# Kernel optimization log

Hardware: AMD Instinct MI355X
Metric: run time of the kernel (lower is better)

The kernel has to match this reference:

```python
import jax, jax.numpy as jnp
import numpy as np

B, C, T, H, W = 2, 512, 8, 16, 16
NUM_HEADS = 8
HEAD_DIM = C // NUM_HEADS


def setup_inputs() -> dict:
    key = jax.random.key(0)
    ks = jax.random.split(key, 6)
    x = jax.random.normal(ks[0], (B, C, T, H, W), dtype=jnp.float32)
    # LayerNorm params
    ln_w = jnp.ones((C,), dtype=jnp.float32)
    ln_b = jnp.zeros((C,), dtype=jnp.float32)
    # 1x1x1 Conv3d == per-token linear; weight stored [out, in]
    w_qkv = jax.random.normal(ks[1], (3 * C, C), dtype=jnp.float32) * (1.0 / np.sqrt(C))
    b_qkv = jnp.zeros((3 * C,), dtype=jnp.float32)
    w_proj = jax.random.normal(ks[2], (C, C), dtype=jnp.float32) * (1.0 / np.sqrt(C))
    b_proj = jnp.zeros((C,), dtype=jnp.float32)
    return {"x": x, "ln_w": ln_w, "ln_b": ln_b, "w_qkv": w_qkv,
            "b_qkv": b_qkv, "w_proj": w_proj, "b_proj": b_proj}


def reference(x, ln_w, ln_b, w_qkv, b_qkv, w_proj, b_proj):
    Bx, Cx, Tx, Hx, Wx = x.shape
    N = Tx * Hx * Wx
    scale = HEAD_DIM ** -0.5

    # [B,C,T,H,W] -> [B,N,C]
    x_flat = jnp.transpose(x, (0, 2, 3, 4, 1)).reshape(Bx, N, Cx)

    # LayerNorm over channels
    mu = jnp.mean(x_flat, axis=-1, keepdims=True)
    var = jnp.var(x_flat, axis=-1, keepdims=True)
    x_flat = (x_flat - mu) * jax.lax.rsqrt(var + 1e-5) * ln_w + ln_b

    # QKV (1x1x1 conv == linear). Output channel layout: [3, heads, head_dim]
    qkv = jnp.einsum('bnc,oc->bno', x_flat, w_qkv) + b_qkv  # [B,N,3C]
    qkv = qkv.reshape(Bx, N, 3, NUM_HEADS, HEAD_DIM)
    qkv = jnp.transpose(qkv, (2, 0, 3, 1, 4))  # [3,B,heads,N,head_dim]
    q, k, v = qkv[0], qkv[1], qkv[2]

    attn = jnp.einsum('bhnd,bhmd->bhnm', q, k) * scale
    attn = jax.nn.softmax(attn, axis=-1)
    x_attn = jnp.einsum('bhnm,bhmd->bhnd', attn, v)  # [B,heads,N,head_dim]
    x_attn = jnp.transpose(x_attn, (0, 2, 1, 3)).reshape(Bx, N, Cx)

    # proj (1x1x1 conv == linear)
    x_attn = jnp.einsum('bnc,oc->bno', x_attn, w_proj) + b_proj

    # NOTE: residual is on the *normalized* x_flat (as in the original module)
    x_out = x_flat + x_attn
    x_out = x_out.reshape(Bx, Tx, Hx, Wx, Cx)
    return jnp.transpose(x_out, (0, 4, 1, 2, 3))  # [B,C,T,H,W]
```

## Files before the change

kernel.cpp:

```cpp
#include <hip/hip_runtime.h>
#include <hip/hip_bf16.h>

#define BB 2
#define CC 512
#define NN 2048
#define NHEADS 8
#define HDIM 64

typedef __attribute__((ext_vector_type(8))) __bf16 bf16x8;
typedef __attribute__((ext_vector_type(4))) __bf16 bf16x4;
typedef __attribute__((ext_vector_type(2))) __bf16 bf16x2;
typedef __attribute__((ext_vector_type(4))) float f32x4;

#define QSCALE 0.18033688f

__global__ __launch_bounds__(256) void ln_stats_kernel(
    const float* __restrict__ x, float* __restrict__ mu, float* __restrict__ rstd) {
  __shared__ float rs[16][16];
  __shared__ float rq[16][16];
  int tl = threadIdx.x & 15;
  int cg = threadIdx.x >> 4;
  int tok = blockIdx.x * 16 + tl;
  int b = tok >> 11;
  int n = tok & (NN - 1);
  const float* xp = x + (size_t)b * CC * NN + n;
  float s = 0.f, ss = 0.f;
  int c0 = cg * 32;
#pragma unroll 8
  for (int c = c0; c < c0 + 32; ++c) {
    float v = xp[(size_t)c * NN];
    s += v;
    ss += v * v;
  }
  rs[cg][tl] = s;
  rq[cg][tl] = ss;
  __syncthreads();
  if (threadIdx.x < 16) {
    int t = threadIdx.x;
    float S = 0.f, SS = 0.f;
#pragma unroll
    for (int gidx = 0; gidx < 16; ++gidx) {
      S += rs[gidx][t];
      SS += rq[gidx][t];
    }
    float m = S * (1.0f / CC);
    float var = SS * (1.0f / CC) - m * m;
    int tk = blockIdx.x * 16 + t;
    mu[tk] = m;
    rstd[tk] = rsqrtf(var + 1e-5f);
  }
}

__global__ __launch_bounds__(256) void ln_transpose_kernel(
    const float* __restrict__ x, const float* __restrict__ mu,
    const float* __restrict__ rstd, const float* __restrict__ lnw,
    const float* __restrict__ lnb, __bf16* __restrict__ xln_t) {
  __shared__ float Xs[64][68];
  int n0 = blockIdx.x * 64;
  int c0 = blockIdx.y * 64;
  int b = blockIdx.z;
  int tid = threadIdx.x;
#pragma unroll
  for (int l = 0; l < 4; ++l) {
    int e = tid + 256 * l;
    int row = e >> 4, c4 = e & 15;
    float4 v = *(const float4*)&x[((size_t)b * CC + c0 + row) * NN + n0 + c4 * 4];
    *(float4*)&Xs[row][c4 * 4] = v;
  }
  __syncthreads();
  int sr = tid >> 2;
  int sc = (tid & 3) * 16;
  int tok = b * NN + n0 + sr;
  float mun = mu[tok], rsn = rstd[tok];
  __bf16 outv[16];
#pragma unroll
  for (int j = 0; j < 16; ++j) {
    int c = c0 + sc + j;
    outv[j] = (__bf16)((Xs[sc + j][sr] - mun) * rsn * lnw[c] + lnb[c]);
  }
  __bf16* dst = &xln_t[((size_t)b * NN + n0 + sr) * CC + c0 + sc];
  *(bf16x8*)&dst[0] = *(bf16x8*)&outv[0];
  *(bf16x8*)&dst[8] = *(bf16x8*)&outv[8];
}

__global__ __launch_bounds__(256) void qkv_mfma_kernel(
    const __bf16* __restrict__ xln_t, const float* __restrict__ w,
    const float* __restrict__ bias, __bf16* __restrict__ qt,
    __bf16* __restrict__ kt, __bf16* __restrict__ vbf) {
  __shared__ __align__(16) __bf16 As[2][64][68];
  __shared__ __align__(16) __bf16 Bs[2][128][68];
  int n0 = blockIdx.x * 128;
  bool swap = blockIdx.y < 16;
  int m0 = swap ? blockIdx.y * 64 : 1024 + ((int)blockIdx.y - 16) * 64;
  int b = blockIdx.z;
  int tid = threadIdx.x;
  int wid = tid >> 6, lane = tid & 63;
  int g = lane >> 4, c = lane & 15;
  int wr = wid >> 1, wc = wid & 1;
  const __bf16* xln = xln_t + (size_t)b * NN * CC;
  int arow = tid >> 4, ac4 = tid & 15;
  int brow = tid >> 3, bc8 = tid & 7;

  float4 wA[4];
  bf16x8 xB[4];
  auto LOADREGS = [&](int k0) {
#pragma unroll
    for (int l = 0; l < 4; ++l)
      wA[l] = *(const float4*)&w[(size_t)(m0 + arow + 16 * l) * CC + k0 + ac4 * 4];
#pragma unroll
    for (int l = 0; l < 4; ++l)
      xB[l] = *(const bf16x8*)&xln[(size_t)(n0 + brow + 32 * l) * CC + k0 + bc8 * 8];
  };
  auto STORELDS = [&](int buf) {
#pragma unroll
    for (int l = 0; l < 4; ++l) {
      bf16x4 pk = {(__bf16)wA[l].x, (__bf16)wA[l].y, (__bf16)wA[l].z,
                   (__bf16)wA[l].w};
      *(bf16x4*)&As[buf][arow + 16 * l][ac4 * 4] = pk;
    }
#pragma unroll
    for (int l = 0; l < 4; ++l)
      *(bf16x8*)&Bs[buf][brow + 32 * l][bc8 * 8] = xB[l];
  };

  LOADREGS(0);
  STORELDS(0);
  __syncthreads();
  f32x4 acc[2][4] = {};
  for (int ktile = 0; ktile < 8; ++ktile) {
    int cur = ktile & 1;
    if (ktile < 7) LOADREGS((ktile + 1) * 64);
#pragma unroll
    for (int hh = 0; hh < 2; ++hh) {
      bf16x8 af[2], bfr[4];
#pragma unroll
      for (int mi = 0; mi < 2; ++mi)
        af[mi] = *(const bf16x8*)&As[cur][wr * 32 + mi * 16 + c][hh * 32 + g * 8];
#pragma unroll
      for (int nj = 0; nj < 4; ++nj)
        bfr[nj] = *(const bf16x8*)&Bs[cur][wc * 64 + nj * 16 + c][hh * 32 + g * 8];
      if (swap) {
#pragma unroll
        for (int mi = 0; mi < 2; ++mi)
#pragma unroll
          for (int nj = 0; nj < 4; ++nj)
            acc[mi][nj] = __builtin_amdgcn_mfma_f32_16x16x32_bf16(
                bfr[nj], af[mi], acc[mi][nj], 0, 0, 0);
      } else {
#pragma unroll
        for (int mi = 0; mi < 2; ++mi)
#pragma unroll
          for (int nj = 0; nj < 4; ++nj)
            acc[mi][nj] = __builtin_amdgcn_mfma_f32_16x16x32_bf16(
                af[mi], bfr[nj], acc[mi][nj], 0, 0, 0);
      }
    }
    if (ktile < 7) STORELDS(cur ^ 1);
    __syncthreads();
  }
  if (swap) {
    int obase = m0 + wr * 32;
    int sec = obase >> 9;
    int osec = obase & 511;
    int head = osec >> 6;
    int dbase = osec & 63;
    __bf16* dst = (sec == 0 ? qt : kt) + (size_t)(b * NHEADS + head) * NN * HDIM;
    float scl = (sec == 0) ? QSCALE : 1.0f;
#pragma unroll
    for (int mi = 0; mi < 2; ++mi) {
      float bo = bias[obase + mi * 16 + c];
      int d = dbase + mi * 16 + c;
#pragma unroll
      for (int nj = 0; nj < 4; ++nj)
#pragma unroll
        for (int r = 0; r < 4; ++r) {
          int n = n0 + wc * 64 + nj * 16 + 4 * g + r;
          dst[(size_t)n * HDIM + d] = (__bf16)((acc[mi][nj][r] + bo) * scl);
        }
    }
  } else {
#pragma unroll
    for (int mi = 0; mi < 2; ++mi)
#pragma unroll
      for (int r = 0; r < 4; ++r) {
        int o = m0 + wr * 32 + mi * 16 + 4 * g + r;
        int ch = o - 1024;
        float bo = bias[o];
#pragma unroll
        for (int nj = 0; nj < 4; ++nj) {
          int n = n0 + wc * 64 + nj * 16 + c;
          vbf[((size_t)b * CC + ch) * NN + n] = (__bf16)(acc[mi][nj][r] + bo);
        }
      }
  }
}

__global__ __launch_bounds__(256, 2) void attn_mfma_kernel(
    const __bf16* __restrict__ qt, const __bf16* __restrict__ ktg,
    const __bf16* __restrict__ vbf, __bf16* __restrict__ xa_t) {
  __shared__ __align__(16) __bf16 Kb[2][64][72];
  __shared__ __align__(16) __bf16 Vb[2][64][72];
  __shared__ __align__(16) __bf16 Ps[64][72];
  int tid = threadIdx.x;
  int wid = tid >> 6, lane = tid & 63;
  int g = lane >> 4, c = lane & 15;
  int n0 = blockIdx.x * 64;
  int h = blockIdx.y, b = blockIdx.z;
  int bh = b * NHEADS + h;
  const __bf16* qbase = qt + ((size_t)bh * NN + n0) * HDIM;
  const __bf16* kbase = ktg + (size_t)bh * NN * HDIM;
  const __bf16* vbase = vbf + ((size_t)b * CC + h * HDIM) * NN;

  int sr = tid >> 2, sc = (tid & 3) * 16;
  bf16x8 kr0 = *(const bf16x8*)(kbase + (size_t)sr * HDIM + sc);
  bf16x8 kr1 = *(const bf16x8*)(kbase + (size_t)sr * HDIM + sc + 8);
  bf16x8 vr0 = *(const bf16x8*)(vbase + (size_t)sr * NN + sc);
  bf16x8 vr1 = *(const bf16x8*)(vbase + (size_t)sr * NN + sc + 8);
  bf16x8 aq0 = *(const bf16x8*)(qbase + (size_t)(wid * 16 + c) * HDIM + g * 8);
  bf16x8 aq1 = *(const bf16x8*)(qbase + (size_t)(wid * 16 + c) * HDIM + 32 + g * 8);
  *(bf16x8*)&Kb[0][sr][sc] = kr0;
  *(bf16x8*)&Kb[0][sr][sc + 8] = kr1;
  *(bf16x8*)&Vb[0][sr][sc] = vr0;
  *(bf16x8*)&Vb[0][sr][sc + 8] = vr1;

  f32x4 O[4] = {};
  float m_ = -1e30f;
  float l_ = 0.f;
  __syncthreads();

  for (int t = 0; t < NN / 64; ++t) {
    int cur = t & 1;
    bool pf = (t + 1 < NN / 64);
    int mt = (t + 1) * 64;
    if (pf) {
      kr0 = *(const bf16x8*)(kbase + (size_t)(mt + sr) * HDIM + sc);
      kr1 = *(const bf16x8*)(kbase + (size_t)(mt + sr) * HDIM + sc + 8);
      vr0 = *(const bf16x8*)(vbase + (size_t)sr * NN + mt + sc);
      vr1 = *(const bf16x8*)(vbase + (size_t)sr * NN + mt + sc + 8);
    }
    f32x4 st[4];
    __builtin_amdgcn_s_setprio(1);
#pragma unroll
    for (int t4 = 0; t4 < 4; ++t4) {
      bf16x8 bk0 = *(const bf16x8*)&Kb[cur][t4 * 16 + c][g * 8];
      bf16x8 bk1 = *(const bf16x8*)&Kb[cur][t4 * 16 + c][32 + g * 8];
      f32x4 acc = {0.f, 0.f, 0.f, 0.f};
      acc = __builtin_amdgcn_mfma_f32_16x16x32_bf16(bk0, aq0, acc, 0, 0, 0);
      acc = __builtin_amdgcn_mfma_f32_16x16x32_bf16(bk1, aq1, acc, 0, 0, 0);
      st[t4] = acc;
    }
    __builtin_amdgcn_s_setprio(0);
    float pm = st[0][0];
#pragma unroll
    for (int t4 = 0; t4 < 4; ++t4)
#pragma unroll
      for (int r = 0; r < 4; ++r) pm = fmaxf(pm, st[t4][r]);
    pm = fmaxf(pm, __shfl_xor(pm, 16));
    pm = fmaxf(pm, __shfl_xor(pm, 32));
    if (!__all(pm <= m_ + 8.0f)) {
      float mn = fmaxf(m_, pm);
      float fs = exp2f(m_ - mn);
      m_ = mn;
      l_ *= fs;
#pragma unroll
      for (int dt = 0; dt < 4; ++dt)
#pragma unroll
        for (int r = 0; r < 4; ++r) O[dt][r] *= fs;
    }
    float ps = 0.f;
#pragma unroll
    for (int t4 = 0; t4 < 4; ++t4) {
      float p0 = exp2f(st[t4][0] - m_);
      float p1 = exp2f(st[t4][1] - m_);
      float p2 = exp2f(st[t4][2] - m_);
      float p3 = exp2f(st[t4][3] - m_);
      ps += (p0 + p1) + (p2 + p3);
      bf16x4 quad = {(__bf16)p0, (__bf16)p1, (__bf16)p2, (__bf16)p3};
      *(bf16x4*)&Ps[wid * 16 + c][t4 * 16 + 4 * g] = quad;
    }
    l_ += ps;
    bf16x8 ap0 = *(const bf16x8*)&Ps[wid * 16 + c][g * 8];
    bf16x8 ap1 = *(const bf16x8*)&Ps[wid * 16 + c][32 + g * 8];
    __builtin_amdgcn_s_setprio(1);
#pragma unroll
    for (int dt = 0; dt < 4; ++dt) {
      bf16x8 bv0 = *(const bf16x8*)&Vb[cur][dt * 16 + c][g * 8];
      bf16x8 bv1 = *(const bf16x8*)&Vb[cur][dt * 16 + c][32 + g * 8];
      O[dt] = __builtin_amdgcn_mfma_f32_16x16x32_bf16(bv0, ap0, O[dt], 0, 0, 0);
      O[dt] = __builtin_amdgcn_mfma_f32_16x16x32_bf16(bv1, ap1, O[dt], 0, 0, 0);
    }
    __builtin_amdgcn_s_setprio(0);
    if (pf) {
      *(bf16x8*)&Kb[cur ^ 1][sr][sc] = kr0;
      *(bf16x8*)&Kb[cur ^ 1][sr][sc + 8] = kr1;
      *(bf16x8*)&Vb[cur ^ 1][sr][sc] = vr0;
      *(bf16x8*)&Vb[cur ^ 1][sr][sc + 8] = vr1;
    }
    __syncthreads();
  }
  float lt = l_ + __shfl_xor(l_, 16);
  lt += __shfl_xor(lt, 32);
  float inv = 1.0f / lt;
  size_t row = (size_t)b * NN + n0 + wid * 16 + c;
#pragma unroll
  for (int dt = 0; dt < 4; ++dt) {
    bf16x4 pk = {(__bf16)(O[dt][0] * inv), (__bf16)(O[dt][1] * inv),
                 (__bf16)(O[dt][2] * inv), (__bf16)(O[dt][3] * inv)};
    *(bf16x4*)&xa_t[row * CC + h * HDIM + dt * 16 + 4 * g] = pk;
  }
}

__global__ __launch_bounds__(256) void proj_mfma_kernel(
    const __bf16* __restrict__ xa_t, const float* __restrict__ w,
    const float* __restrict__ bias, const float* __restrict__ x,
    const float* __restrict__ mu, const float* __restrict__ rstd,
    const float* __restrict__ lnw, const float* __restrict__ lnb,
    float* __restrict__ out) {
  __shared__ __align__(16) __bf16 As[2][64][68];
  __shared__ __align__(16) __bf16 Bs[2][64][68];
  int n0 = blockIdx.x * 64;
  int m0 = blockIdx.y * 64;
  int b = blockIdx.z;
  int tid = threadIdx.x;
  int wid = tid >> 6, lane = tid & 63;
  int g = lane >> 4, c = lane & 15;
  int wr = wid >> 1, wc = wid & 1;
  const __bf16* xab = xa_t + (size_t)b * NN * CC;
  int arow = tid >> 4, ac4 = tid & 15;
  int brow = tid >> 3, bc8 = tid & 7;

  float4 wA[4];
  bf16x8 xB[2];
  auto LOADREGS = [&](int k0) {
#pragma unroll
    for (int l = 0; l < 4; ++l)
      wA[l] = *(const float4*)&w[(size_t)(m0 + arow + 16 * l) * CC + k0 + ac4 * 4];
#pragma unroll
    for (int l = 0; l < 2; ++l)
      xB[l] = *(const bf16x8*)&xab[(size_t)(n0 + brow + 32 * l) * CC + k0 + bc8 * 8];
  };
  auto STORELDS = [&](int buf) {
#pragma unroll
    for (int l = 0; l < 4; ++l) {
      bf16x4 pk = {(__bf16)wA[l].x, (__bf16)wA[l].y, (__bf16)wA[l].z,
                   (__bf16)wA[l].w};
      *(bf16x4*)&As[buf][arow + 16 * l][ac4 * 4] = pk;
    }
#pragma unroll
    for (int l = 0; l < 2; ++l)
      *(bf16x8*)&Bs[buf][brow + 32 * l][bc8 * 8] = xB[l];
  };

  LOADREGS(0);
  STORELDS(0);
  __syncthreads();
  f32x4 acc[2][2] = {};
  for (int ktile = 0; ktile < 8; ++ktile) {
    int cur = ktile & 1;
    if (ktile < 7) LOADREGS((ktile + 1) * 64);
#pragma unroll
    for (int hh = 0; hh < 2; ++hh) {
      bf16x8 af[2], bfr[2];
#pragma unroll
      for (int mi = 0; mi < 2; ++mi)
        af[mi] = *(const bf16x8*)&As[cur][wr * 32 + mi * 16 + c][hh * 32 + g * 8];
#pragma unroll
      for (int nj = 0; nj < 2; ++nj)
        bfr[nj] = *(const bf16x8*)&Bs[cur][wc * 32 + nj * 16 + c][hh * 32 + g * 8];
#pragma unroll
      for (int mi = 0; mi < 2; ++mi)
#pragma unroll
        for (int nj = 0; nj < 2; ++nj)
          acc[mi][nj] = __builtin_amdgcn_mfma_f32_16x16x32_bf16(
              af[mi], bfr[nj], acc[mi][nj], 0, 0, 0);
    }
    if (ktile < 7) STORELDS(cur ^ 1);
    __syncthreads();
  }
#pragma unroll
  for (int mi = 0; mi < 2; ++mi)
#pragma unroll
    for (int r = 0; r < 4; ++r) {
      int o = m0 + wr * 32 + mi * 16 + 4 * g + r;
      float bo = bias[o], gw = lnw[o], gb = lnb[o];
#pragma unroll
      for (int nj = 0; nj < 2; ++nj) {
        int n = n0 + wc * 32 + nj * 16 + c;
        int tok = b * NN + n;
        float xv = x[((size_t)b * CC + o) * NN + n];
        float xlnv = (xv - mu[tok]) * rstd[tok] * gw + gb;
        out[((size_t)b * CC + o) * NN + n] = acc[mi][nj][r] + bo + xlnv;
      }
    }
}

extern "C" void kernel_launch(void* const* d_in, const int* in_sizes, int n_in,
                              void* d_out, int out_size, void* d_ws, size_t ws_size,
                              hipStream_t stream) {
  const float* x = (const float*)d_in[0];
  const float* lnw = (const float*)d_in[1];
  const float* lnb = (const float*)d_in[2];
  const float* wqkv = (const float*)d_in[3];
  const float* bqkv = (const float*)d_in[4];
  const float* wproj = (const float*)d_in[5];
  const float* bproj = (const float*)d_in[6];
  float* out = (float*)d_out;
  (void)in_sizes; (void)n_in; (void)out_size; (void)ws_size;

  char* wsb = (char*)d_ws;
  float* mu = (float*)wsb;
  float* rstd = mu + 4096;
  const size_t HSZ = (size_t)BB * NHEADS * NN * HDIM;
  __bf16* qt = (__bf16*)(wsb + 32768);
  __bf16* kt = qt + HSZ;
  __bf16* vbf = kt + HSZ;
  __bf16* xln_t = vbf + HSZ;
  __bf16* xa_t = xln_t + HSZ;

  hipLaunchKernelGGL(ln_stats_kernel, dim3(256), dim3(256), 0, stream, x, mu, rstd);
  hipLaunchKernelGGL(ln_transpose_kernel, dim3(32, 8, 2), dim3(256), 0, stream,
                     x, mu, rstd, lnw, lnb, xln_t);
  hipLaunchKernelGGL(qkv_mfma_kernel, dim3(16, 24, 2), dim3(256), 0, stream,
                     xln_t, wqkv, bqkv, qt, kt, vbf);
  hipLaunchKernelGGL(attn_mfma_kernel, dim3(32, 8, 2), dim3(256), 0, stream,
                     qt, kt, vbf, xa_t);
  hipLaunchKernelGGL(proj_mfma_kernel, dim3(32, 8, 2), dim3(256), 0, stream,
                     xa_t, wproj, bproj, x, mu, rstd, lnw, lnb, out);
}
```

Baseline: 79.52 us.

## Split attention KV range across blocks and merge with a combine kernel

The attention kernel now uses 512-thread blocks covering 128 query rows, and splits the 2048 keys into two halves handled by separate blocks (flash-decoding style). Each block writes unnormalized fp32 partial outputs plus its running max and sum. A new combine kernel rescales and merges the two halves into the bf16 attention output. The aim is more parallel work and shorter serial loops per block, at the cost of an extra launch and the fp32 partial-output traffic through global memory.

```diff
diff --git a/kernel.cpp b/kernel.cpp
--- a/kernel.cpp
+++ b/kernel.cpp
@@ -6,6 +6,8 @@
 #define NN 2048
 #define NHEADS 8
 #define HDIM 64
+#define NSPLIT 2
+#define KVHALF 1024
 
 typedef __attribute__((ext_vector_type(8))) __bf16 bf16x8;
 typedef __attribute__((ext_vector_type(4))) __bf16 bf16x4;
@@ -195,48 +197,44 @@
   }
 }
 
-__global__ __launch_bounds__(256, 2) void attn_mfma_kernel(
+__global__ __launch_bounds__(512, 4) void attn_mfma_kernel(
     const __bf16* __restrict__ qt, const __bf16* __restrict__ ktg,
-    const __bf16* __restrict__ vbf, __bf16* __restrict__ xa_t) {
+    const __bf16* __restrict__ vbf, float* __restrict__ opart,
+    float* __restrict__ ml) {
   __shared__ __align__(16) __bf16 Kb[2][64][72];
   __shared__ __align__(16) __bf16 Vb[2][64][72];
-  __shared__ __align__(16) __bf16 Ps[64][72];
+  __shared__ __align__(16) __bf16 Ps[128][72];
   int tid = threadIdx.x;
   int wid = tid >> 6, lane = tid & 63;
   int g = lane >> 4, c = lane & 15;
-  int n0 = blockIdx.x * 64;
-  int h = blockIdx.y, b = blockIdx.z;
+  int n0 = blockIdx.x * 128;
+  int h = blockIdx.y;
+  int b = blockIdx.z >> 1, split = blockIdx.z & 1;
   int bh = b * NHEADS + h;
   const __bf16* qbase = qt + ((size_t)bh * NN + n0) * HDIM;
-  const __bf16* kbase = ktg + (size_t)bh * NN * HDIM;
-  const __bf16* vbase = vbf + ((size_t)b * CC + h * HDIM) * NN;
-
-  int sr = tid >> 2, sc = (tid & 3) * 16;
-  bf16x8 kr0 = *(const bf16x8*)(kbase + (size_t)sr * HDIM + sc);
-  bf16x8 kr1 = *(const bf16x8*)(kbase + (size_t)sr * HDIM + sc + 8);
-  bf16x8 vr0 = *(const bf16x8*)(vbase + (size_t)sr * NN + sc);
-  bf16x8 vr1 = *(const bf16x8*)(vbase + (size_t)sr * NN + sc + 8);
+  const __bf16* kbase = ktg + ((size_t)bh * NN + split * KVHALF) * HDIM;
+  const __bf16* vbase = vbf + ((size_t)b * CC + h * HDIM) * NN + split * KVHALF;
+
+  int sr = tid >> 3, sc = (tid & 7) * 8;
+  bf16x8 kr = *(const bf16x8*)(kbase + (size_t)sr * HDIM + sc);
+  bf16x8 vr = *(const bf16x8*)(vbase + (size_t)sr * NN + sc);
   bf16x8 aq0 = *(const bf16x8*)(qbase + (size_t)(wid * 16 + c) * HDIM + g * 8);
   bf16x8 aq1 = *(const bf16x8*)(qbase + (size_t)(wid * 16 + c) * HDIM + 32 + g * 8);
-  *(bf16x8*)&Kb[0][sr][sc] = kr0;
-  *(bf16x8*)&Kb[0][sr][sc + 8] = kr1;
-  *(bf16x8*)&Vb[0][sr][sc] = vr0;
-  *(bf16x8*)&Vb[0][sr][sc + 8] = vr1;
+  *(bf16x8*)&Kb[0][sr][sc] = kr;
+  *(bf16x8*)&Vb[0][sr][sc] = vr;
 
   f32x4 O[4] = {};
   float m_ = -1e30f;
   float l_ = 0.f;
   __syncthreads();
 
-  for (int t = 0; t < NN / 64; ++t) {
+  for (int t = 0; t < KVHALF / 64; ++t) {
     int cur = t & 1;
-    bool pf = (t + 1 < NN / 64);
+    bool pf = (t + 1 < KVHALF / 64);
     int mt = (t + 1) * 64;
     if (pf) {
-      kr0 = *(const bf16x8*)(kbase + (size_t)(mt + sr) * HDIM + sc);
-      kr1 = *(const bf16x8*)(kbase + (size_t)(mt + sr) * HDIM + sc + 8);
-      vr0 = *(const bf16x8*)(vbase + (size_t)sr * NN + mt + sc);
-      vr1 = *(const bf16x8*)(vbase + (size_t)sr * NN + mt + sc + 8);
+      kr = *(const bf16x8*)(kbase + (size_t)(mt + sr) * HDIM + sc);
+      vr = *(const bf16x8*)(vbase + (size_t)sr * NN + mt + sc);
     }
     f32x4 st[4];
     __builtin_amdgcn_s_setprio(1);
@@ -291,23 +289,47 @@
     }
     __builtin_amdgcn_s_setprio(0);
     if (pf) {
-      *(bf16x8*)&Kb[cur ^ 1][sr][sc] = kr0;
-      *(bf16x8*)&Kb[cur ^ 1][sr][sc + 8] = kr1;
-      *(bf16x8*)&Vb[cur ^ 1][sr][sc] = vr0;
-      *(bf16x8*)&Vb[cur ^ 1][sr][sc + 8] = vr1;
+      *(bf16x8*)&Kb[cur ^ 1][sr][sc] = kr;
+      *(bf16x8*)&Vb[cur ^ 1][sr][sc] = vr;
     }
     __syncthreads();
   }
   float lt = l_ + __shfl_xor(l_, 16);
   lt += __shfl_xor(lt, 32);
-  float inv = 1.0f / lt;
-  size_t row = (size_t)b * NN + n0 + wid * 16 + c;
-#pragma unroll
-  for (int dt = 0; dt < 4; ++dt) {
-    bf16x4 pk = {(__bf16)(O[dt][0] * inv), (__bf16)(O[dt][1] * inv),
-                 (__bf16)(O[dt][2] * inv), (__bf16)(O[dt][3] * inv)};
-    *(bf16x4*)&xa_t[row * CC + h * HDIM + dt * 16 + 4 * g] = pk;
-  }
+  size_t prow = ((size_t)(split * BB + b) * NHEADS + h) * NN + (n0 + wid * 16 + c);
+#pragma unroll
+  for (int dt = 0; dt < 4; ++dt)
+    *(f32x4*)&opart[prow * HDIM + dt * 16 + 4 * g] = O[dt];
+  if (lane < 16) {
+    float2 mlv = {m_, lt};
+    *(float2*)&ml[prow * 2] = mlv;
+  }
+}
+
+__global__ __launch_bounds__(256) void attn_combine_kernel(
+    const float* __restrict__ opart, const float* __restrict__ ml,
+    __bf16* __restrict__ xa_t) {
+  int t = threadIdx.x;
+  int row_local = t >> 4;
+  int dq = (t & 15) * 4;
+  int R = blockIdx.x * 16 + row_local;
+  int n = R & (NN - 1);
+  int bh = R >> 11;
+  int b = bh >> 3, h = bh & 7;
+  size_t p0 = ((size_t)(0 * BB + b) * NHEADS + h) * NN + n;
+  size_t p1 = ((size_t)(1 * BB + b) * NHEADS + h) * NN + n;
+  float m0 = ml[p0 * 2], l0 = ml[p0 * 2 + 1];
+  float m1 = ml[p1 * 2], l1 = ml[p1 * 2 + 1];
+  float m = fmaxf(m0, m1);
+  float w0 = exp2f(m0 - m), w1 = exp2f(m1 - m);
+  float linv = 1.0f / (l0 * w0 + l1 * w1);
+  float4 o0 = *(const float4*)&opart[p0 * HDIM + dq];
+  float4 o1 = *(const float4*)&opart[p1 * HDIM + dq];
+  bf16x4 pk = {(__bf16)((o0.x * w0 + o1.x * w1) * linv),
+               (__bf16)((o0.y * w0 + o1.y * w1) * linv),
+               (__bf16)((o0.z * w0 + o1.z * w1) * linv),
+               (__bf16)((o0.w * w0 + o1.w * w1) * linv)};
+  *(bf16x4*)&xa_t[((size_t)b * NN + n) * CC + h * HDIM + dq] = pk;
 }
 
 __global__ __launch_bounds__(256) void proj_mfma_kernel(
@@ -414,16 +436,21 @@
   __bf16* qt = (__bf16*)(wsb + 32768);
   __bf16* kt = qt + HSZ;
   __bf16* vbf = kt + HSZ;
-  __bf16* xln_t = vbf + HSZ;
-  __bf16* xa_t = xln_t + HSZ;
+  __bf16* xa_t = vbf + HSZ;
+  __bf16* xln_t = xa_t + HSZ;
+  float* opart = (float*)xln_t;
+  float* ml = (float*)(wsb + 32768 + 4 * HSZ * sizeof(__bf16) +
+                       (size_t)NSPLIT * HSZ * sizeof(float));
 
   hipLaunchKernelGGL(ln_stats_kernel, dim3(256), dim3(256), 0, stream, x, mu, rstd);
   hipLaunchKernelGGL(ln_transpose_kernel, dim3(32, 8, 2), dim3(256), 0, stream,
                      x, mu, rstd, lnw, lnb, xln_t);
   hipLaunchKernelGGL(qkv_mfma_kernel, dim3(16, 24, 2), dim3(256), 0, stream,
                      xln_t, wqkv, bqkv, qt, kt, vbf);
-  hipLaunchKernelGGL(attn_mfma_kernel, dim3(32, 8, 2), dim3(256), 0, stream,
-                     qt, kt, vbf, xa_t);
+  hipLaunchKernelGGL(attn_mfma_kernel, dim3(16, 8, 4), dim3(512), 0, stream,
+                     qt, kt, vbf, opart, ml);
+  hipLaunchKernelGGL(attn_combine_kernel, dim3(2048), dim3(256), 0, stream,
+                     opart, ml, xa_t);
   hipLaunchKernelGGL(proj_mfma_kernel, dim3(32, 8, 2), dim3(256), 0, stream,
                      xa_t, wproj, bproj, x, mu, rstd, lnw, lnb, out);
 }
```

Result: no change. 80.04 us (+0.7%).
